# Optimization experiments

Hardware: AMD Instinct MI355X
Metric: run time of the kernel (lower is better)

## Reference

```python
import jax, jax.numpy as jnp
import numpy as np

N_NODES = 75000
N_EDGES = 1200000
DIM = 64


def setup_inputs() -> dict:
    key = jax.random.key(0)
    ks = jax.random.split(key, 9)
    d_u = jax.random.normal(ks[0], (N_NODES, DIM), dtype=jnp.float32)
    p_u = jax.random.normal(ks[1], (N_NODES, DIM), dtype=jnp.float32)
    s = 1.0 / np.sqrt(DIM)
    w_q = jax.random.normal(ks[2], (DIM, DIM), dtype=jnp.float32) * s
    w_k = jax.random.normal(ks[3], (DIM, DIM), dtype=jnp.float32) * s
    w_v = jax.random.normal(ks[4], (DIM, DIM), dtype=jnp.float32) * s
    e1 = jax.random.normal(ks[5], (DIM,), dtype=jnp.float32) * s
    e2 = jax.random.normal(ks[6], (DIM,), dtype=jnp.float32) * s
    src = jax.random.randint(ks[7], (N_EDGES,), 0, N_NODES, dtype=jnp.int32)
    dst = jax.random.randint(ks[8], (N_EDGES,), 0, N_NODES, dtype=jnp.int32)
    return {"d_u": d_u, "p_u": p_u, "w_q": w_q, "w_k": w_k, "w_v": w_v,
            "e1": e1, "e2": e2, "src": src, "dst": dst}


def reference(d_u, p_u, w_q, w_k, w_v, e1, e2, src, dst):
    n_nodes = d_u.shape[0]
    # per-node edge scores: e1(w_k(p_u)) on src side, e2(w_q(d_u)) on dst side
    h_src = (p_u @ w_k.T) @ e1            # [N]
    h_dst = (d_u @ w_q.T) @ e2            # [N]
    # apply_edges(u_add_v): c_e = h_src[u] + h_dst[v], shape [E]
    c = h_src[src] + h_dst[dst]
    # EdgeWeightNorm(norm='right'): divide by sum of incoming edge weights at dst
    denom = jax.ops.segment_sum(c, dst, num_segments=n_nodes)  # [N]
    c = c / denom[dst]
    # update_all(u_mul_e, sum): messages w_v(p_u)[u] * c_e, summed at dst
    wv = p_u @ w_v.T                      # [N, D]
    msg = wv[src] * c[:, None]            # [E, D]
    out = jax.ops.segment_sum(msg, dst, num_segments=n_nodes)  # [N, D]
    return out
```

## Files before the change

### kernel.cpp

```cpp
#include <hip/hip_runtime.h>

#define N_NODES 75000
#define N_EDGES 1200000
#define DIM 64
#define SCAN_BLK 1024
#define N_SCAN_BLKS ((N_NODES + SCAN_BLK - 1) / SCAN_BLK)
#define NCOPY 8
#define HIST_BLKS ((N_EDGES + 1023) / 1024)

__device__ __forceinline__ float lane_bcf(float v, int l) {
    return __int_as_float(__builtin_amdgcn_readlane(__float_as_int(v), l));
}
__device__ __forceinline__ int lane_bci(int v, int l) {
    return __builtin_amdgcn_readlane(v, l);
}

__global__ void vec_precompute(const float* __restrict__ w_q,
                               const float* __restrict__ w_k,
                               const float* __restrict__ e1,
                               const float* __restrict__ e2,
                               double* __restrict__ a,
                               double* __restrict__ b) {
    int t = threadIdx.x;
    if (t < DIM) {
        double s = 0.0;
        #pragma unroll
        for (int j = 0; j < DIM; ++j) s += (double)e1[j] * (double)w_k[j * DIM + t];
        a[t] = s;
    } else if (t < 2 * DIM) {
        int d = t - DIM;
        double s = 0.0;
        #pragma unroll
        for (int j = 0; j < DIM; ++j) s += (double)e2[j] * (double)w_q[j * DIM + d];
        b[d] = s;
    }
}

__global__ __launch_bounds__(256, 4) void node_wave(
    const float* __restrict__ d_u, const float* __restrict__ p_u,
    const float* __restrict__ w_v,
    const double* __restrict__ a_vec, const double* __restrict__ b_vec,
    double* __restrict__ h_src, double* __restrict__ h_dst,
    float* __restrict__ wv_out) {
    int lane = threadIdx.x & 63;
    int wave = (blockIdx.x * 256 + threadIdx.x) >> 6;
    int nwaves = gridDim.x * 4;

    float w[DIM];
    const float4* wr = (const float4*)(w_v + (size_t)lane * DIM);
    #pragma unroll
    for (int k = 0; k < DIM / 4; ++k) {
        float4 v = wr[k];
        w[4 * k + 0] = v.x; w[4 * k + 1] = v.y;
        w[4 * k + 2] = v.z; w[4 * k + 3] = v.w;
    }
    double al = a_vec[lane];
    double bl = b_vec[lane];

    for (int i = wave; i < N_NODES; i += nwaves) {
        float pl = p_u[(size_t)i * DIM + lane];
        float dl = d_u[(size_t)i * DIM + lane];

        double hs = (double)pl * al;
        #pragma unroll
        for (int off = 32; off > 0; off >>= 1) hs += __shfl_xor(hs, off, 64);
        double hd = (double)dl * bl;
        #pragma unroll
        for (int off = 32; off > 0; off >>= 1) hd += __shfl_xor(hd, off, 64);
        if (lane == 0) { h_src[i] = hs; h_dst[i] = hd; }

        float a0 = 0.f, a1 = 0.f, a2 = 0.f, a3 = 0.f;
        #pragma unroll
        for (int d = 0; d < DIM; d += 4) {
            a0 += w[d + 0] * lane_bcf(pl, d + 0);
            a1 += w[d + 1] * lane_bcf(pl, d + 1);
            a2 += w[d + 2] * lane_bcf(pl, d + 2);
            a3 += w[d + 3] * lane_bcf(pl, d + 3);
        }
        wv_out[(size_t)i * DIM + lane] = (a0 + a1) + (a2 + a3);
    }
}

__global__ __launch_bounds__(256) void hist_kernel(
    const int* __restrict__ dst, int* __restrict__ cnt8,
    int* __restrict__ rank) {
    int base = blockIdx.x << 10;
    int* mycnt = cnt8 + (size_t)(blockIdx.x & (NCOPY - 1)) * N_NODES;
    #pragma unroll
    for (int k = 0; k < 4; ++k) {
        int e = base + k * 256 + threadIdx.x;
        if (e < N_EDGES) rank[e] = atomicAdd(&mycnt[dst[e]], 1);
    }
}

__global__ __launch_bounds__(SCAN_BLK) void scan1_kernel(
    int* __restrict__ cnt8, int* __restrict__ cnt,
    int* __restrict__ row, int* __restrict__ bsum) {
    __shared__ int sh[SCAN_BLK];
    int tid = threadIdx.x;
    int i = blockIdx.x * SCAN_BLK + tid;
    int v = 0;
    if (i < N_NODES) {
        int run = 0;
        #pragma unroll
        for (int c = 0; c < NCOPY; ++c) {
            int x = cnt8[(size_t)c * N_NODES + i];
            cnt8[(size_t)c * N_NODES + i] = run;
            run += x;
        }
        v = run;
        cnt[i] = run;
    }
    sh[tid] = v;
    __syncthreads();
    for (int off = 1; off < SCAN_BLK; off <<= 1) {
        int t = (tid >= off) ? sh[tid - off] : 0;
        __syncthreads();
        sh[tid] += t;
        __syncthreads();
    }
    if (i < N_NODES) row[i] = sh[tid] - v;
    if (tid == SCAN_BLK - 1) bsum[blockIdx.x] = sh[tid];
}

__global__ __launch_bounds__(256) void scan23_kernel(
    int* __restrict__ row, const int* __restrict__ bsum) {
    __shared__ int pref[N_SCAN_BLKS];
    int tid = threadIdx.x;
    if (tid == 0) {
        int run = 0;
        #pragma unroll 8
        for (int k = 0; k < N_SCAN_BLKS; ++k) { pref[k] = run; run += bsum[k]; }
    }
    __syncthreads();
    int i = blockIdx.x * 256 + tid;
    if (i >= N_NODES) return;
    row[i] += pref[i / SCAN_BLK];
}

__global__ __launch_bounds__(256) void build_kernel(
    const int* __restrict__ src, const int* __restrict__ dst,
    const int* __restrict__ row, const int* __restrict__ cnt8,
    const int* __restrict__ rank, int* __restrict__ csr_src) {
    int e = blockIdx.x * 256 + threadIdx.x;
    if (e >= N_EDGES) return;
    int d = dst[e];
    int copy = (e >> 10) & (NCOPY - 1);
    int pos = row[d] + cnt8[(size_t)copy * N_NODES + d] + rank[e];
    csr_src[pos] = src[e];
}

__global__ __launch_bounds__(256) void node_gather(
    const int* __restrict__ row, const int* __restrict__ cnt,
    const int* __restrict__ csr_src,
    const double* __restrict__ h_src, const double* __restrict__ h_dst,
    const float* __restrict__ wv, float* __restrict__ out) {
    int gtid = blockIdx.x * 256 + threadIdx.x;
    int node = gtid >> 6;
    int lane = threadIdx.x & 63;
    if (node >= N_NODES) return;

    int start = row[node];
    int deg = cnt[node];
    double hd = h_dst[node];

    if (deg <= 64) {
        int s0 = 0;
        double c0 = 0.0;
        if (lane < deg) {
            s0 = csr_src[start + lane];
            c0 = h_src[s0] + hd;
        }
        double r = c0;
        #pragma unroll
        for (int off = 32; off > 0; off >>= 1) r += __shfl_xor(r, off, 64);
        double inv = 1.0 / r;
        float cf0 = (lane < deg) ? (float)(c0 * inv) : 0.f;

        float acc = 0.f;
        int j = 0;
        for (; j + 4 <= deg; j += 4) {
            int sA = lane_bci(s0, j + 0); float cA = lane_bcf(cf0, j + 0);
            int sB = lane_bci(s0, j + 1); float cB = lane_bcf(cf0, j + 1);
            int sC = lane_bci(s0, j + 2); float cC = lane_bcf(cf0, j + 2);
            int sD = lane_bci(s0, j + 3); float cD = lane_bcf(cf0, j + 3);
            float wA = wv[(size_t)sA * DIM + lane];
            float wB = wv[(size_t)sB * DIM + lane];
            float wC = wv[(size_t)sC * DIM + lane];
            float wD = wv[(size_t)sD * DIM + lane];
            acc += wA * cA;
            acc += wB * cB;
            acc += wC * cC;
            acc += wD * cD;
        }
        for (; j < deg; ++j) {
            int s = lane_bci(s0, j); float cf = lane_bcf(cf0, j);
            acc += wv[(size_t)s * DIM + lane] * cf;
        }
        out[(size_t)node * DIM + lane] = acc;
    } else {
        double denom = 0.0;
        for (int base = 0; base < deg; base += 64) {
            int m = deg - base; if (m > 64) m = 64;
            double c = 0.0;
            if (lane < m) {
                int s = csr_src[start + base + lane];
                c = h_src[s] + hd;
            }
            #pragma unroll
            for (int off = 32; off > 0; off >>= 1) c += __shfl_xor(c, off, 64);
            denom += c;
        }
        double inv = 1.0 / denom;
        float acc = 0.f;
        for (int base = 0; base < deg; base += 64) {
            int m = deg - base; if (m > 64) m = 64;
            int s1 = 0; float cf1 = 0.f;
            if (lane < m) {
                s1 = csr_src[start + base + lane];
                cf1 = (float)((h_src[s1] + hd) * inv);
            }
            for (int j = 0; j < m; ++j) {
                int s = lane_bci(s1, j);
                float cf = lane_bcf(cf1, j);
                acc += wv[(size_t)s * DIM + lane] * cf;
            }
        }
        out[(size_t)node * DIM + lane] = acc;
    }
}

extern "C" void kernel_launch(void* const* d_in, const int* in_sizes, int n_in,
                              void* d_out, int out_size, void* d_ws, size_t ws_size,
                              hipStream_t stream) {
    const float* d_u = (const float*)d_in[0];
    const float* p_u = (const float*)d_in[1];
    const float* w_q = (const float*)d_in[2];
    const float* w_k = (const float*)d_in[3];
    const float* w_v = (const float*)d_in[4];
    const float* e1  = (const float*)d_in[5];
    const float* e2  = (const float*)d_in[6];
    const int*   src = (const int*)d_in[7];
    const int*   dst = (const int*)d_in[8];
    float* out = (float*)d_out;

    double* a      = (double*)d_ws;
    double* b      = a + DIM;
    double* h_src  = b + DIM;
    double* h_dst  = h_src + N_NODES;
    float*  wv     = (float*)(h_dst + N_NODES);
    int*    cnt    = (int*)(wv + (size_t)N_NODES * DIM);
    int*    row    = cnt + N_NODES;
    int*    bsum   = row + N_NODES;
    int*    cnt8   = bsum + 128;
    int*    rank   = cnt8 + (size_t)NCOPY * N_NODES;
    int*    csr_src= rank + N_EDGES;

    vec_precompute<<<1, 128, 0, stream>>>(w_q, w_k, e1, e2, a, b);

    hipMemsetAsync(cnt8, 0, sizeof(int) * (size_t)NCOPY * N_NODES, stream);

    hist_kernel<<<HIST_BLKS, 256, 0, stream>>>(dst, cnt8, rank);

    node_wave<<<1024, 256, 0, stream>>>(
        d_u, p_u, w_v, a, b, h_src, h_dst, wv);

    scan1_kernel<<<N_SCAN_BLKS, SCAN_BLK, 0, stream>>>(cnt8, cnt, row, bsum);
    scan23_kernel<<<(N_NODES + 255) / 256, 256, 0, stream>>>(row, bsum);

    build_kernel<<<(N_EDGES + 255) / 256, 256, 0, stream>>>(
        src, dst, row, cnt8, rank, csr_src);

    node_gather<<<(N_NODES * 64 + 255) / 256, 256, 0, stream>>>(
        row, cnt, csr_src, h_src, h_dst, wv, out);
}
```

Baseline: 265.6 us.

## Drop rank array via atomic CSR fill and gather four edges per wave with float4

The histogram kernel no longer stores a per-edge rank. Instead, the build kernel reuses the per-copy scanned offsets as atomic cursors to place each source index, which removes a 1.2M-int write and read. The low-degree gather path now splits the wave into four 16-lane groups that each load a whole 64-float row as float4 and handle a different edge, then reduces across groups with shuffles. Its denominator reduction also skips shuffle stages when the degree is small. In exchange, the build kernel takes on extra atomic contention, and the edge order within each CSR row becomes nondeterministic, which makes float summation order vary between runs.

Result: slower. 299.1 us (+12.6%).

```diff
diff --git a/kernel.cpp b/kernel.cpp
--- a/kernel.cpp
+++ b/kernel.cpp
@@ -82,14 +82,13 @@
 }
 
 __global__ __launch_bounds__(256) void hist_kernel(
-    const int* __restrict__ dst, int* __restrict__ cnt8,
-    int* __restrict__ rank) {
+    const int* __restrict__ dst, int* __restrict__ cnt8) {
     int base = blockIdx.x << 10;
     int* mycnt = cnt8 + (size_t)(blockIdx.x & (NCOPY - 1)) * N_NODES;
     #pragma unroll
     for (int k = 0; k < 4; ++k) {
         int e = base + k * 256 + threadIdx.x;
-        if (e < N_EDGES) rank[e] = atomicAdd(&mycnt[dst[e]], 1);
+        if (e < N_EDGES) atomicAdd(&mycnt[dst[e]], 1);
     }
 }
 
@@ -140,14 +139,19 @@
 
 __global__ __launch_bounds__(256) void build_kernel(
     const int* __restrict__ src, const int* __restrict__ dst,
-    const int* __restrict__ row, const int* __restrict__ cnt8,
-    const int* __restrict__ rank, int* __restrict__ csr_src) {
-    int e = blockIdx.x * 256 + threadIdx.x;
-    if (e >= N_EDGES) return;
-    int d = dst[e];
-    int copy = (e >> 10) & (NCOPY - 1);
-    int pos = row[d] + cnt8[(size_t)copy * N_NODES + d] + rank[e];
-    csr_src[pos] = src[e];
+    const int* __restrict__ row, int* __restrict__ cnt8,
+    int* __restrict__ csr_src) {
+    int base = blockIdx.x << 10;
+    int* mycnt = cnt8 + (size_t)(blockIdx.x & (NCOPY - 1)) * N_NODES;
+    #pragma unroll
+    for (int k = 0; k < 4; ++k) {
+        int e = base + k * 256 + threadIdx.x;
+        if (e < N_EDGES) {
+            int d = dst[e];
+            int pos = row[d] + atomicAdd(&mycnt[d], 1);
+            csr_src[pos] = src[e];
+        }
+    }
 }
 
 __global__ __launch_bounds__(256) void node_gather(
@@ -172,32 +176,47 @@
             c0 = h_src[s0] + hd;
         }
         double r = c0;
-        #pragma unroll
-        for (int off = 32; off > 0; off >>= 1) r += __shfl_xor(r, off, 64);
+        if (deg > 32) r += __shfl_xor(r, 32, 64);
+        if (deg > 16) r += __shfl_xor(r, 16, 64);
+        r += __shfl_xor(r, 8, 64);
+        r += __shfl_xor(r, 4, 64);
+        r += __shfl_xor(r, 2, 64);
+        r += __shfl_xor(r, 1, 64);
         double inv = 1.0 / r;
         float cf0 = (lane < deg) ? (float)(c0 * inv) : 0.f;
 
-        float acc = 0.f;
+        int g = lane >> 4;
+        int sub = lane & 15;
+        float ax = 0.f, ay = 0.f, az = 0.f, aw = 0.f;
+        int rounds = (deg + 3) >> 2;
         int j = 0;
-        for (; j + 4 <= deg; j += 4) {
-            int sA = lane_bci(s0, j + 0); float cA = lane_bcf(cf0, j + 0);
-            int sB = lane_bci(s0, j + 1); float cB = lane_bcf(cf0, j + 1);
-            int sC = lane_bci(s0, j + 2); float cC = lane_bcf(cf0, j + 2);
-            int sD = lane_bci(s0, j + 3); float cD = lane_bcf(cf0, j + 3);
-            float wA = wv[(size_t)sA * DIM + lane];
-            float wB = wv[(size_t)sB * DIM + lane];
-            float wC = wv[(size_t)sC * DIM + lane];
-            float wD = wv[(size_t)sD * DIM + lane];
-            acc += wA * cA;
-            acc += wB * cB;
-            acc += wC * cC;
-            acc += wD * cD;
-        }
-        for (; j < deg; ++j) {
-            int s = lane_bci(s0, j); float cf = lane_bcf(cf0, j);
-            acc += wv[(size_t)s * DIM + lane] * cf;
-        }
-        out[(size_t)node * DIM + lane] = acc;
+        for (; j + 2 <= rounds; j += 2) {
+            int l0 = 4 * j + g;
+            int l1 = l0 + 4;
+            int   sA = __shfl(s0, l0, 64);
+            float cA = __shfl(cf0, l0, 64);
+            int   sB = __shfl(s0, l1, 64);
+            float cB = __shfl(cf0, l1, 64);
+            float4 vA = ((const float4*)(wv + (size_t)sA * DIM))[sub];
+            float4 vB = ((const float4*)(wv + (size_t)sB * DIM))[sub];
+            ax += vA.x * cA; ay += vA.y * cA; az += vA.z * cA; aw += vA.w * cA;
+            ax += vB.x * cB; ay += vB.y * cB; az += vB.z * cB; aw += vB.w * cB;
+        }
+        if (j < rounds) {
+            int l0 = 4 * j + g;
+            int   sA = __shfl(s0, l0, 64);
+            float cA = __shfl(cf0, l0, 64);
+            float4 vA = ((const float4*)(wv + (size_t)sA * DIM))[sub];
+            ax += vA.x * cA; ay += vA.y * cA; az += vA.z * cA; aw += vA.w * cA;
+        }
+        ax += __shfl_xor(ax, 16, 64); ay += __shfl_xor(ay, 16, 64);
+        az += __shfl_xor(az, 16, 64); aw += __shfl_xor(aw, 16, 64);
+        ax += __shfl_xor(ax, 32, 64); ay += __shfl_xor(ay, 32, 64);
+        az += __shfl_xor(az, 32, 64); aw += __shfl_xor(aw, 32, 64);
+        if (g == 0) {
+            float4 o; o.x = ax; o.y = ay; o.z = az; o.w = aw;
+            ((float4*)(out + (size_t)node * DIM))[sub] = o;
+        }
     } else {
         double denom = 0.0;
         for (int base = 0; base < deg; base += 64) {
@@ -253,14 +272,13 @@
     int*    row    = cnt + N_NODES;
     int*    bsum   = row + N_NODES;
     int*    cnt8   = bsum + 128;
-    int*    rank   = cnt8 + (size_t)NCOPY * N_NODES;
-    int*    csr_src= rank + N_EDGES;
+    int*    csr_src= cnt8 + (size_t)NCOPY * N_NODES;
 
     vec_precompute<<<1, 128, 0, stream>>>(w_q, w_k, e1, e2, a, b);
 
     hipMemsetAsync(cnt8, 0, sizeof(int) * (size_t)NCOPY * N_NODES, stream);
 
-    hist_kernel<<<HIST_BLKS, 256, 0, stream>>>(dst, cnt8, rank);
+    hist_kernel<<<HIST_BLKS, 256, 0, stream>>>(dst, cnt8);
 
     node_wave<<<1024, 256, 0, stream>>>(
         d_u, p_u, w_v, a, b, h_src, h_dst, wv);
@@ -268,8 +286,8 @@
     scan1_kernel<<<N_SCAN_BLKS, SCAN_BLK, 0, stream>>>(cnt8, cnt, row, bsum);
     scan23_kernel<<<(N_NODES + 255) / 256, 256, 0, stream>>>(row, bsum);
 
-    build_kernel<<<(N_EDGES + 255) / 256, 256, 0, stream>>>(
-        src, dst, row, cnt8, rank, csr_src);
+    build_kernel<<<HIST_BLKS, 256, 0, stream>>>(
+        src, dst, row, cnt8, csr_src);
 
     node_gather<<<(N_NODES * 64 + 255) / 256, 256, 0, stream>>>(
         row, cnt, csr_src, h_src, h_dst, wv, out);
```
